# Performance work log

Measured on AMD Instinct MI355X. Metric: run time of the kernel, lower is better.

## Reference

```python
import jax, jax.numpy as jnp
import numpy as np
from jax import lax

VOCAB, ENC_DIM, PRED_H, JOINT_H = 4096, 1024, 640, 640
T, MAX_SYM, BLANK, SOS = 128, 30, 0, -1
S = T * (MAX_SYM + 1)  # upper bound on greedy-decode loop iterations


def setup_inputs() -> dict:
    key = jax.random.key(0)
    ks = jax.random.split(key, 10)
    rn = lambda k, shape, s: jax.random.normal(k, shape, jnp.float32) * s
    return {
        "enc_out": rn(ks[0], (1, T, ENC_DIM), 1.0),
        "out_len": T,
        "emb": rn(ks[1], (VOCAB, PRED_H), 0.1),
        "Wih0": rn(ks[2], (4 * PRED_H, PRED_H), 0.04),
        "Whh0": rn(ks[3], (4 * PRED_H, PRED_H), 0.04),
        "b0": jnp.zeros((4 * PRED_H,), jnp.float32),
        "Wih1": rn(ks[4], (4 * PRED_H, PRED_H), 0.04),
        "Whh1": rn(ks[5], (4 * PRED_H, PRED_H), 0.04),
        "b1": jnp.zeros((4 * PRED_H,), jnp.float32),
        "Wj1": rn(ks[6], (JOINT_H, ENC_DIM + PRED_H), 0.03),
        "bj1": jnp.zeros((JOINT_H,), jnp.float32),
        "Wj2": rn(ks[7], (VOCAB, JOINT_H), 0.04),
        "bj2": jnp.zeros((VOCAB,), jnp.float32),
    }


def _lstm_cell(x, h, c, Wih, Whh, b):
    z = x @ Wih.T + h @ Whh.T + b  # [4H], torch gate order i,f,g,o
    i, f, g, o = jnp.split(z, 4)
    c2 = jax.nn.sigmoid(f) * c + jax.nn.sigmoid(i) * jnp.tanh(g)
    return jax.nn.sigmoid(o) * jnp.tanh(c2), c2


def _decode(enc_out, timesteps, emb, Wih0, Whh0, b0, Wih1, Whh1, b1, Wj1, bj1, Wj2, bj2):
    enc = enc_out[0]  # [T, ENC_DIM]

    def step(carry, _):
        t, sa, last, h0, c0, h1, c1, labels, cnt, done = carry
        # prediction net step (SOS = -1 -> zero embedding)
        g_in = jnp.where(last < 0, 0.0, emb[jnp.maximum(last, 0)])
        h0n, c0n = _lstm_cell(g_in, h0, c0, Wih0, Whh0, b0)
        h1n, c1n = _lstm_cell(h0n, h1, c1, Wih1, Whh1, b1)
        # joint net on current encoder frame
        f = enc[jnp.minimum(t, T - 1)]
        hid = jax.nn.relu(Wj1 @ jnp.concatenate([f, h1n]) + bj1)
        logits = Wj2 @ hid + bj2  # [VOCAB]
        k = jnp.argmax(logits).astype(jnp.int32)
        stop_sym = (k == BLANK) | (sa >= MAX_SYM)
        emit = (~stop_sym) & (~done)
        adv = stop_sym & (~done)
        # emit: append symbol, keep hidden'; blank/max: advance time, discard hidden'
        last2 = jnp.where(emit, k, last)
        h0 = jnp.where(emit, h0n, h0); c0 = jnp.where(emit, c0n, c0)
        h1 = jnp.where(emit, h1n, h1); c1 = jnp.where(emit, c1n, c1)
        labels = labels.at[cnt].set(jnp.where(emit, k, labels[cnt]))
        cnt2 = cnt + emit.astype(jnp.int32)
        sa2 = jnp.where(emit, sa + 1, jnp.where(adv, 0, sa))
        t2 = t + adv.astype(jnp.int32)
        done2 = done | (adv & (t2 >= timesteps))
        out_logits = jnp.where(done, 0.0, logits)
        return (t2, sa2, last2, h0, c0, h1, c1, labels, cnt2, done2), out_logits

    zeros = jnp.zeros((PRED_H,), jnp.float32)
    carry0 = (jnp.int32(0), jnp.int32(0), jnp.int32(SOS),
              zeros, zeros, zeros, zeros,
              jnp.full((S,), -1, jnp.int32), jnp.int32(0), jnp.bool_(False))
    carry, logits_seq = lax.scan(step, carry0, None, length=S)
    labels, cnt = carry[7], carry[8]
    return logits_seq, labels, cnt


def reference(enc_out, out_len, emb, Wih0, Whh0, b0, Wih1, Whh1, b1, Wj1, bj1, Wj2, bj2):
    return _decode(enc_out, out_len, emb, Wih0, Whh0, b0, Wih1, Whh1, b1, Wj1, bj1, Wj2, bj2)
```

## Files before the change

kernel.cpp:

```cpp
#include <hip/hip_runtime.h>
#include <cmath>

#define VOCAB   4096
#define ENC_DIM 1024
#define PRED_H  640
#define JOINT_H 640
#define TMAX    128
#define MAX_SYM 30
#define NSTEPS  (TMAX*(MAX_SYM+1))
#define NWG     160
#define NTHR    512
#define RLX __ATOMIC_RELAXED
#define AGT __HIP_MEMORY_SCOPE_AGENT

typedef unsigned long long u64;
typedef __attribute__((ext_vector_type(4))) float f32x4;


__device__ __forceinline__ float wave_red(float v){
  v += __shfl_xor(v, 32, 64);
  v += __shfl_xor(v, 16, 64);
  v += __shfl_xor(v,  8, 64);
  v += __shfl_xor(v,  4, 64);
  v += __shfl_xor(v,  2, 64);
  v += __shfl_xor(v,  1, 64);
  return v;
}

__device__ __forceinline__ float sigf(float x){ return 1.0f/(1.0f+expf(-x)); }

__device__ __forceinline__ void hop_send(float* data, unsigned* flag, int w,
                                         f32x4 v, unsigned tag){
  asm volatile("global_store_dwordx4 %0, %1, off sc0 sc1"
               :: "v"(data + (w<<4)), "v"(v) : "memory");
  asm volatile("s_waitcnt vmcnt(0)" ::: "memory");
  __hip_atomic_store(flag + (w<<4), tag, RLX, AGT);
}

__device__ __forceinline__ void hop_recv(const unsigned* flag, const float* data,
                                         float* dstLDS, unsigned tag, int i){
  const unsigned* fp = flag + (i<<4);
  for(;;){
    unsigned f;
    asm volatile("global_load_dword %0, %1, off sc0 sc1\n\ts_waitcnt vmcnt(0)"
                 : "=v"(f) : "v"(fp) : "memory");
    if (f >= tag) break;
    __builtin_amdgcn_s_sleep(2);
  }
  f32x4 v;
  asm volatile("global_load_dwordx4 %0, %1, off sc0 sc1\n\ts_waitcnt vmcnt(0)"
               : "=v"(v) : "v"(data + (i<<4)) : "memory");
  __builtin_amdgcn_sched_barrier(0);
  *(f32x4*)&dstLDS[i<<2] = v;
}

__device__ __forceinline__ u64 mkentry(float lg, int r, unsigned ep){
  unsigned u = __float_as_uint(lg);
  u = (u & 0x80000000u) ? ~u : (u | 0x80000000u);
  return ((u64)u<<24) | ((u64)(ep&0xFFFu)<<12) | (u64)(4095 - r);
}

__global__ void init_ws(unsigned* ws){
  for (int i = threadIdx.x; i < 18432; i += 256) ws[i] = 0u;
}

__global__ __launch_bounds__(NTHR, 2)
void rnnt_decode(const float* __restrict__ enc,
                 const int*   __restrict__ outlen_p,
                 const float* __restrict__ emb,
                 const float* __restrict__ Wih0, const float* __restrict__ Whh0, const float* __restrict__ b0,
                 const float* __restrict__ Wih1, const float* __restrict__ Whh1, const float* __restrict__ b1,
                 const float* __restrict__ Wj1,  const float* __restrict__ bj1,
                 const float* __restrict__ Wj2,  const float* __restrict__ bj2,
                 float* __restrict__ out,
                 char* __restrict__ ws)
{
  const int wg = blockIdx.x, tid = threadIdx.x;
  const int wave = tid >> 6, lane = tid & 63;
  const int timesteps = outlen_p[0];

  unsigned* flagA = (unsigned*)(ws);
  unsigned* flagB = (unsigned*)(ws + 10240);
  unsigned* flagH = (unsigned*)(ws + 20480);
  float*    dataA = (float*)   (ws + 30720);
  float*    dataB = (float*)   (ws + 40960);
  float*    dataH = (float*)   (ws + 51200);
  u64*      parts = (u64*)     (ws + 61440);

  __shared__ float xa[PRED_H];
  __shared__ float xsh[ENC_DIM];
  __shared__ float h0buf[2][PRED_H];
  __shared__ float h1buf[2][PRED_H];
  __shared__ float hidsh[JOINT_H];
  __shared__ float zsh[4][4];
  __shared__ float zjsA[8], zjsB[8];
  __shared__ float c0c[4], c1c[4], c0p[4], c1p[4];
  __shared__ float bj1sh[4];
  __shared__ u64 psh[8];
  __shared__ u64 pmx[3];

  const int jb = wg*4;

  const int gA = wave & 3;
  const int jA = wave >> 2;
  const int rowA = gA*PRED_H + jb + jA;
  const int rowB = gA*PRED_H + jb + jA + 2;

  float w0xA[10], w0hA[10], w0xB[10], w0hB[10];
  float w1xA[10], w1hA[10], w1xB[10], w1hB[10];
  #pragma unroll
  for (int i = 0; i < 10; ++i){
    int c = lane + (i<<6);
    w0xA[i] = Wih0[(size_t)rowA*PRED_H + c];
    w0hA[i] = Whh0[(size_t)rowA*PRED_H + c];
    w1xA[i] = Wih1[(size_t)rowA*PRED_H + c];
    w1hA[i] = Whh1[(size_t)rowA*PRED_H + c];
    w0xB[i] = Wih0[(size_t)rowB*PRED_H + c];
    w0hB[i] = Whh0[(size_t)rowB*PRED_H + c];
    w1xB[i] = Wih1[(size_t)rowB*PRED_H + c];
    w1hB[i] = Whh1[(size_t)rowB*PRED_H + c];
  }
  const float bA0 = b0[rowA], bA1 = b1[rowA];
  const float bB0 = b0[rowB], bB1 = b1[rowB];

  const int grp = wave >> 2;
  const int vt  = ((wave & 3)<<6) | lane;
  const int rP0 = jb + grp;
  const int rP1 = jb + 2 + grp;
  float wjf0[4], wjh0[3], wjf1[4], wjh1[3];
  #pragma unroll
  for (int i = 0; i < 4; ++i){
    wjf0[i] = Wj1[(size_t)rP0*(ENC_DIM+PRED_H) + vt + (i<<8)];
    wjf1[i] = Wj1[(size_t)rP1*(ENC_DIM+PRED_H) + vt + (i<<8)];
  }
  #pragma unroll
  for (int i = 0; i < 3; ++i){
    int c = vt + (i<<8);
    wjh0[i] = (c < PRED_H) ? Wj1[(size_t)rP0*(ENC_DIM+PRED_H) + ENC_DIM + c] : 0.f;
    wjh1[i] = (c < PRED_H) ? Wj1[(size_t)rP1*(ENC_DIM+PRED_H) + ENC_DIM + c] : 0.f;
  }
  float ca0 = 0.f, ca1 = 0.f;

  const int nrows = (wg < 96) ? 26 : 25;
  const int r2b = wg*25 + (wg < 96 ? wg : 96);
  float wj2[4][10], bj2r[4];
  #pragma unroll
  for (int p = 0; p < 4; ++p){
    bool act = (p*8 + wave) < nrows;
    int r = act ? (r2b + p*8 + wave) : 0;
    #pragma unroll
    for (int i = 0; i < 10; ++i)
      wj2[p][i] = act ? Wj2[(size_t)r*JOINT_H + lane + (i<<6)] : 0.f;
    bj2r[p] = act ? bj2[r] : 0.f;
  }

  for (int i = tid; i < PRED_H; i += NTHR){ h0buf[0][i] = 0.f; h1buf[0][i] = 0.f; }
  if (tid < 4){ c0c[tid] = 0.f; c1c[tid] = 0.f; bj1sh[tid] = bj1[jb+tid]; }
  __syncthreads();

  int cur = 0, t = 0, sa = 0, last = -1, cnt = 0, tStaged = -1;
  bool done = false, reuse = false;

  for (int s = 0; s < NSTEPS; ++s){
    if (done){
      if (wg < 8) out[(size_t)s*VOCAB + wg*NTHR + tid] = 0.f;
      continue;
    }
    const unsigned tag = (unsigned)(s + 1);

    if (!reuse){
      for (int i = tid; i < PRED_H; i += NTHR)
        xa[i] = (last >= 0) ? emb[(size_t)last*PRED_H + i] : 0.f;
      __syncthreads();
      {
        float acc = 0.f;
        #pragma unroll
        for (int i = 0; i < 10; ++i) acc = fmaf(w0xA[i], xa[lane+(i<<6)], acc);
        #pragma unroll
        for (int i = 0; i < 10; ++i) acc = fmaf(w0hA[i], h0buf[cur][lane+(i<<6)], acc);
        acc = wave_red(acc);
        if (lane == 0) zsh[gA][jA] = acc + bA0;
        float a2 = 0.f;
        #pragma unroll
        for (int i = 0; i < 10; ++i) a2 = fmaf(w0xB[i], xa[lane+(i<<6)], a2);
        #pragma unroll
        for (int i = 0; i < 10; ++i) a2 = fmaf(w0hB[i], h0buf[cur][lane+(i<<6)], a2);
        a2 = wave_red(a2);
        if (lane == 0) zsh[gA][jA+2] = a2 + bB0;
      }
      __syncthreads();
      if (wave == 0){
        float hv = 0.f;
        if (lane < 4){
          float ig = sigf(zsh[0][lane]), fg = sigf(zsh[1][lane]);
          float gg = tanhf(zsh[2][lane]), og = sigf(zsh[3][lane]);
          float c2 = fg*c0c[lane] + ig*gg;
          c0p[lane] = c2;
          hv = og*tanhf(c2);
        }
        f32x4 v;
        v.x = __shfl(hv, 0, 64); v.y = __shfl(hv, 1, 64);
        v.z = __shfl(hv, 2, 64); v.w = __shfl(hv, 3, 64);
        if (lane == 0) hop_send(dataA, flagA, wg, v, tag);
      }

      if (tid < 160) hop_recv(flagA, dataA, h0buf[cur^1], tag, tid);
      __syncthreads();
      {
        float acc = 0.f;
        #pragma unroll
        for (int i = 0; i < 10; ++i) acc = fmaf(w1xA[i], h0buf[cur^1][lane+(i<<6)], acc);
        #pragma unroll
        for (int i = 0; i < 10; ++i) acc = fmaf(w1hA[i], h1buf[cur][lane+(i<<6)], acc);
        acc = wave_red(acc);
        if (lane == 0) zsh[gA][jA] = acc + bA1;
        float a2 = 0.f;
        #pragma unroll
        for (int i = 0; i < 10; ++i) a2 = fmaf(w1xB[i], h0buf[cur^1][lane+(i<<6)], a2);
        #pragma unroll
        for (int i = 0; i < 10; ++i) a2 = fmaf(w1hB[i], h1buf[cur][lane+(i<<6)], a2);
        a2 = wave_red(a2);
        if (lane == 0) zsh[gA][jA+2] = a2 + bB1;
      }
      __syncthreads();
      if (wave == 0){
        float hv = 0.f;
        if (lane < 4){
          float ig = sigf(zsh[0][lane]), fg = sigf(zsh[1][lane]);
          float gg = tanhf(zsh[2][lane]), og = sigf(zsh[3][lane]);
          float c2 = fg*c1c[lane] + ig*gg;
          c1p[lane] = c2;
          hv = og*tanhf(c2);
        }
        f32x4 v;
        v.x = __shfl(hv, 0, 64); v.y = __shfl(hv, 1, 64);
        v.z = __shfl(hv, 2, 64); v.w = __shfl(hv, 3, 64);
        if (lane == 0) hop_send(dataB, flagB, wg, v, tag);
      }
    }

    {
      int tcap = (t < TMAX-1) ? t : (TMAX-1);
      bool fNew = (tcap != tStaged);
      if (fNew)
        for (int i = tid; i < ENC_DIM; i += NTHR) xsh[i] = enc[(size_t)tcap*ENC_DIM + i];
      if (!reuse){
        if (tid < 160) hop_recv(flagB, dataB, h1buf[cur^1], tag, tid);
      }
      __syncthreads();
      if (fNew){
        float a = 0.f, b = 0.f;
        #pragma unroll
        for (int i = 0; i < 4; ++i){
          a = fmaf(wjf0[i], xsh[vt+(i<<8)], a);
          b = fmaf(wjf1[i], xsh[vt+(i<<8)], b);
        }
        ca0 = a; ca1 = b;
        tStaged = tcap;
      }
      {
        float acc = ca0;
        #pragma unroll
        for (int i = 0; i < 3; ++i){
          int c = vt + (i<<8);
          acc = fmaf(wjh0[i], h1buf[cur^1][(c < PRED_H) ? c : 0], acc);
        }
        acc = wave_red(acc);
        if (lane == 0) zjsA[wave] = acc;
        float acc2 = ca1;
        #pragma unroll
        for (int i = 0; i < 3; ++i){
          int c = vt + (i<<8);
          acc2 = fmaf(wjh1[i], h1buf[cur^1][(c < PRED_H) ? c : 0], acc2);
        }
        acc2 = wave_red(acc2);
        if (lane == 0) zjsB[wave] = acc2;
      }
      __syncthreads();
      if (wave == 0){
        float hv = 0.f;
        if (lane < 4){
          float v;
          if (lane == 0)      v = zjsA[0]+zjsA[1]+zjsA[2]+zjsA[3] + bj1sh[0];
          else if (lane == 1) v = zjsA[4]+zjsA[5]+zjsA[6]+zjsA[7] + bj1sh[1];
          else if (lane == 2) v = zjsB[0]+zjsB[1]+zjsB[2]+zjsB[3] + bj1sh[2];
          else                v = zjsB[4]+zjsB[5]+zjsB[6]+zjsB[7] + bj1sh[3];
          hv = v > 0.f ? v : 0.f;
        }
        f32x4 v;
        v.x = __shfl(hv, 0, 64); v.y = __shfl(hv, 1, 64);
        v.z = __shfl(hv, 2, 64); v.w = __shfl(hv, 3, 64);
        if (lane == 0) hop_send(dataH, flagH, wg, v, tag);
      }
    }

    int k;
    {
      if (tid < 160) hop_recv(flagH, dataH, hidsh, tag, tid);
      __syncthreads();
      u64 best = 0;
      #pragma unroll
      for (int p = 0; p < 4; ++p){
        if (p*8 + wave < nrows){
          int r = r2b + p*8 + wave;
          float acc = 0.f;
          #pragma unroll
          for (int i = 0; i < 10; ++i) acc = fmaf(wj2[p][i], hidsh[lane+(i<<6)], acc);
          acc = wave_red(acc);
          if (lane == 0){
            float lg = acc + bj2r[p];
            out[(size_t)s*VOCAB + r] = lg;
            u64 e = mkentry(lg, r, tag);
            if (e > best) best = e;
          }
        }
      }
      if (lane == 0) psh[wave] = best;
      __syncthreads();
      if (tid == 0){
        u64 m = psh[0];
        #pragma unroll
        for (int w = 1; w < 8; ++w) if (psh[w] > m) m = psh[w];
        __hip_atomic_store(&parts[(size_t)wg<<3], m, RLX, AGT);
      }
      u64 myp = 0;
      if (tid < 160){
        for(;;){
          u64 e = __hip_atomic_load(&parts[(size_t)tid<<3], RLX, AGT);
          if ((unsigned)((e>>12) & 0xFFFu) == (tag & 0xFFFu)){ myp = e; break; }
          __builtin_amdgcn_s_sleep(2);
        }
      }
      if (wave < 3){
        #pragma unroll
        for (int off = 32; off; off >>= 1){
          u64 o = __shfl_xor(myp, off, 64);
          if (o > myp) myp = o;
        }
        if (lane == 0) pmx[wave] = myp;
      }
      __syncthreads();
      u64 m = pmx[0];
      if (pmx[1] > m) m = pmx[1];
      if (pmx[2] > m) m = pmx[2];
      k = 4095 - (int)(m & 0xFFFull);
    }

    bool stop = (k == 0) || (sa >= MAX_SYM);
    if (!stop){
      if (wg == 0 && tid == 0) out[(size_t)NSTEPS*VOCAB + cnt] = (float)k;
      if (tid < 4){ c0c[tid] = c0p[tid]; c1c[tid] = c1p[tid]; }
      cnt++; sa++; last = k; cur ^= 1; reuse = false;
    } else {
      sa = 0; t++; reuse = true;
      if (t >= timesteps) done = true;
    }
    __syncthreads();
  }

  size_t lab = (size_t)NSTEPS*VOCAB;
  int gidx = wg*NTHR + tid;
  for (int i = cnt + gidx; i < NSTEPS; i += NWG*NTHR) out[lab + i] = -1.f;
  if (wg == 0 && tid == 0) out[lab + NSTEPS] = (float)cnt;
}

extern "C" void kernel_launch(void* const* d_in, const int* in_sizes, int n_in,
                              void* d_out, int out_size, void* d_ws, size_t ws_size,
                              hipStream_t stream) {
  const float* enc  = (const float*)d_in[0];
  const int*   olen = (const int*)  d_in[1];
  const float* emb  = (const float*)d_in[2];
  const float* Wih0 = (const float*)d_in[3];
  const float* Whh0 = (const float*)d_in[4];
  const float* b0   = (const float*)d_in[5];
  const float* Wih1 = (const float*)d_in[6];
  const float* Whh1 = (const float*)d_in[7];
  const float* b1   = (const float*)d_in[8];
  const float* Wj1  = (const float*)d_in[9];
  const float* bj1  = (const float*)d_in[10];
  const float* Wj2  = (const float*)d_in[11];
  const float* bj2  = (const float*)d_in[12];
  float* out = (float*)d_out;
  char* ws = (char*)d_ws;

  init_ws<<<1, 256, 0, stream>>>((unsigned*)d_ws);

  void* args[] = {&enc,&olen,&emb,&Wih0,&Whh0,&b0,&Wih1,&Whh1,&b1,
                  &Wj1,&bj1,&Wj2,&bj2,&out,&ws};
  hipLaunchCooperativeKernel((const void*)rnnt_decode, dim3(NWG), dim3(NTHR),
                             args, 0, stream);
}
```

Baseline: 47.38 ms.

## Embed tags in data words to replace flag-then-data handshake

Each cross-workgroup hop now packs the four hidden values with a copy of the step tag next to every value, written as two 16-byte stores with no wait and no separate flag store. Receivers poll the data line itself and accept it once all tag words match, which removes one store/wait/flag round trip on the sender and one dependent load on the receiver per hop. Poll sleep intervals are also shortened. The risk is that correctness relies on each 8-byte value/tag pair being written and seen atomically, and the sleep change adds polling traffic.

```diff
diff --git a/kernel.cpp b/kernel.cpp
--- a/kernel.cpp
+++ b/kernel.cpp
@@ -15,6 +15,7 @@
 
 typedef unsigned long long u64;
 typedef __attribute__((ext_vector_type(4))) float f32x4;
+typedef __attribute__((ext_vector_type(4))) unsigned int u32x4;
 
 
 __device__ __forceinline__ float wave_red(float v){
@@ -29,29 +30,34 @@
 
 __device__ __forceinline__ float sigf(float x){ return 1.0f/(1.0f+expf(-x)); }
 
-__device__ __forceinline__ void hop_send(float* data, unsigned* flag, int w,
-                                         f32x4 v, unsigned tag){
-  asm volatile("global_store_dwordx4 %0, %1, off sc0 sc1"
-               :: "v"(data + (w<<4)), "v"(v) : "memory");
-  asm volatile("s_waitcnt vmcnt(0)" ::: "memory");
-  __hip_atomic_store(flag + (w<<4), tag, RLX, AGT);
-}
-
-__device__ __forceinline__ void hop_recv(const unsigned* flag, const float* data,
-                                         float* dstLDS, unsigned tag, int i){
-  const unsigned* fp = flag + (i<<4);
+__device__ __forceinline__ void sendline(u64* base, int w, f32x4 hv, unsigned tag){
+  u32x4 a, b;
+  a.x = __float_as_uint(hv.x); a.y = tag; a.z = __float_as_uint(hv.y); a.w = tag;
+  b.x = __float_as_uint(hv.z); b.y = tag; b.z = __float_as_uint(hv.w); b.w = tag;
+  u64* p = base + ((size_t)w<<3);
+  asm volatile("global_store_dwordx4 %0, %2, off sc0 sc1\n\t"
+               "global_store_dwordx4 %1, %3, off sc0 sc1"
+               :: "v"(p), "v"(p+2), "v"(a), "v"(b) : "memory");
+}
+
+__device__ __forceinline__ void pollline(const u64* base, float* dstLDS,
+                                         unsigned tag, int i){
+  const u64* p = base + ((size_t)i<<3);
+  u32x4 v0, v1;
   for(;;){
-    unsigned f;
-    asm volatile("global_load_dword %0, %1, off sc0 sc1\n\ts_waitcnt vmcnt(0)"
-                 : "=v"(f) : "v"(fp) : "memory");
-    if (f >= tag) break;
-    __builtin_amdgcn_s_sleep(2);
-  }
-  f32x4 v;
-  asm volatile("global_load_dwordx4 %0, %1, off sc0 sc1\n\ts_waitcnt vmcnt(0)"
-               : "=v"(v) : "v"(data + (i<<4)) : "memory");
+    asm volatile("global_load_dwordx4 %0, %2, off sc0 sc1\n\t"
+                 "global_load_dwordx4 %1, %3, off sc0 sc1\n\t"
+                 "s_waitcnt vmcnt(0)"
+                 : "=&v"(v0), "=&v"(v1) : "v"(p), "v"(p+2) : "memory");
+    if (v0.y == tag && v0.w == tag && v1.y == tag && v1.w == tag) break;
+    __builtin_amdgcn_s_sleep(1);
+  }
   __builtin_amdgcn_sched_barrier(0);
-  *(f32x4*)&dstLDS[i<<2] = v;
+  float* d = dstLDS + (i<<2);
+  d[0] = __uint_as_float(v0.x);
+  d[1] = __uint_as_float(v0.z);
+  d[2] = __uint_as_float(v1.x);
+  d[3] = __uint_as_float(v1.z);
 }
 
 __device__ __forceinline__ u64 mkentry(float lg, int r, unsigned ep){
@@ -61,7 +67,7 @@
 }
 
 __global__ void init_ws(unsigned* ws){
-  for (int i = threadIdx.x; i < 18432; i += 256) ws[i] = 0u;
+  for (int i = threadIdx.x; i < 10240; i += 256) ws[i] = 0u;
 }
 
 __global__ __launch_bounds__(NTHR, 2)
@@ -79,13 +85,10 @@
   const int wave = tid >> 6, lane = tid & 63;
   const int timesteps = outlen_p[0];
 
-  unsigned* flagA = (unsigned*)(ws);
-  unsigned* flagB = (unsigned*)(ws + 10240);
-  unsigned* flagH = (unsigned*)(ws + 20480);
-  float*    dataA = (float*)   (ws + 30720);
-  float*    dataB = (float*)   (ws + 40960);
-  float*    dataH = (float*)   (ws + 51200);
-  u64*      parts = (u64*)     (ws + 61440);
+  u64* dataA = (u64*)(ws);
+  u64* dataB = (u64*)(ws + 10240);
+  u64* dataH = (u64*)(ws + 20480);
+  u64* parts = (u64*)(ws + 30720);
 
   __shared__ float xa[PRED_H];
   __shared__ float xsh[ENC_DIM];
@@ -201,10 +204,10 @@
         f32x4 v;
         v.x = __shfl(hv, 0, 64); v.y = __shfl(hv, 1, 64);
         v.z = __shfl(hv, 2, 64); v.w = __shfl(hv, 3, 64);
-        if (lane == 0) hop_send(dataA, flagA, wg, v, tag);
-      }
-
-      if (tid < 160) hop_recv(flagA, dataA, h0buf[cur^1], tag, tid);
+        if (lane == 0) sendline(dataA, wg, v, tag);
+      }
+
+      if (tid < 160) pollline(dataA, h0buf[cur^1], tag, tid);
       __syncthreads();
       {
         float acc = 0.f;
@@ -235,7 +238,7 @@
         f32x4 v;
         v.x = __shfl(hv, 0, 64); v.y = __shfl(hv, 1, 64);
         v.z = __shfl(hv, 2, 64); v.w = __shfl(hv, 3, 64);
-        if (lane == 0) hop_send(dataB, flagB, wg, v, tag);
+        if (lane == 0) sendline(dataB, wg, v, tag);
       }
     }
 
@@ -245,7 +248,7 @@
       if (fNew)
         for (int i = tid; i < ENC_DIM; i += NTHR) xsh[i] = enc[(size_t)tcap*ENC_DIM + i];
       if (!reuse){
-        if (tid < 160) hop_recv(flagB, dataB, h1buf[cur^1], tag, tid);
+        if (tid < 160) pollline(dataB, h1buf[cur^1], tag, tid);
       }
       __syncthreads();
       if (fNew){
@@ -290,13 +293,13 @@
         f32x4 v;
         v.x = __shfl(hv, 0, 64); v.y = __shfl(hv, 1, 64);
         v.z = __shfl(hv, 2, 64); v.w = __shfl(hv, 3, 64);
-        if (lane == 0) hop_send(dataH, flagH, wg, v, tag);
+        if (lane == 0) sendline(dataH, wg, v, tag);
       }
     }
 
     int k;
     {
-      if (tid < 160) hop_recv(flagH, dataH, hidsh, tag, tid);
+      if (tid < 160) pollline(dataH, hidsh, tag, tid);
       __syncthreads();
       u64 best = 0;
       #pragma unroll
@@ -328,7 +331,7 @@
         for(;;){
           u64 e = __hip_atomic_load(&parts[(size_t)tid<<3], RLX, AGT);
           if ((unsigned)((e>>12) & 0xFFFu) == (tag & 0xFFFu)){ myp = e; break; }
-          __builtin_amdgcn_s_sleep(2);
+          __builtin_amdgcn_s_sleep(1);
         }
       }
       if (wave < 3){
```

New measurement: 50.17 ms. 5.9% more time.
